# Kernel optimization log

Hardware: AMD Instinct MI355X
Metric: run time of the kernel (lower is better)

Reference implementation:

```python
import jax, jax.numpy as jnp
import numpy as np

N_NODES = 8192
SEQ = 256
H = 32  # lstm_hdim == gcn_hdim


def lstm_layer(x, Wih, Whh, bih, bhh, return_seq):
    # x: [B, S, D] -> torch nn.LSTM, gate order i,f,g,o
    B = x.shape[0]
    Hd = Whh.shape[1]
    b = bih + bhh

    def step(carry, xt):
        h, c = carry
        z = xt @ Wih.T + h @ Whh.T + b  # [B, 4H]
        i, f, g, o = jnp.split(z, 4, axis=-1)
        c = jax.nn.sigmoid(f) * c + jax.nn.sigmoid(i) * jnp.tanh(g)
        h = jax.nn.sigmoid(o) * jnp.tanh(c)
        return (h, c), (h if return_seq else None)

    init = (jnp.zeros((B, Hd), x.dtype), jnp.zeros((B, Hd), x.dtype))
    (h_n, _), ys = jax.lax.scan(step, init, jnp.transpose(x, (1, 0, 2)))
    if return_seq:
        ys = jnp.transpose(ys, (1, 0, 2))  # [B, S, H]
    return ys, h_n


def layer_norm(x, g, b, eps=1e-5):
    mu = jnp.mean(x, axis=-1, keepdims=True)
    var = jnp.mean((x - mu) ** 2, axis=-1, keepdims=True)
    return (x - mu) * jax.lax.rsqrt(var + eps) * g + b


def gcn_conv(x, edge_index, edge_weight, W, bias, n_nodes):
    # PyG GCNConv with self-loops (fill 1.0) and symmetric normalization.
    h = x @ W  # transform first (in_dim -> out_dim)
    src, dst = edge_index[0], edge_index[1]
    deg = jax.ops.segment_sum(edge_weight, dst, num_segments=n_nodes) + 1.0  # +1 self loop
    dinv = jnp.where(deg > 0, jax.lax.rsqrt(deg), 0.0)
    norm = dinv[src] * edge_weight * dinv[dst]  # [E]
    agg = jax.ops.segment_sum(norm[:, None] * h[src], dst, num_segments=n_nodes)
    agg = agg + h * (dinv * dinv)[:, None]  # self-loop message
    return agg + bias


def setup_inputs() -> dict:
    key = jax.random.key(0)
    ks = jax.random.split(key, 20)
    s = 0.1
    d = {
        "x": jax.random.normal(ks[0], (N_NODES, SEQ), jnp.float32),
        "edge_weight": jax.random.uniform(ks[1], (262144,), jnp.float32),
        "Wih1": jax.random.normal(ks[2], (4 * H, 1)) * s,
        "Whh1": jax.random.normal(ks[3], (4 * H, H)) * s,
        "bih1": jax.random.normal(ks[4], (4 * H,)) * s,
        "bhh1": jax.random.normal(ks[5], (4 * H,)) * s,
        "ln1_g": jnp.ones((H,), jnp.float32),
        "ln1_b": jnp.zeros((H,), jnp.float32),
        "Wih2": jax.random.normal(ks[6], (4 * H, H)) * s,
        "Whh2": jax.random.normal(ks[7], (4 * H, H)) * s,
        "bih2": jax.random.normal(ks[8], (4 * H,)) * s,
        "bhh2": jax.random.normal(ks[9], (4 * H,)) * s,
        "Wg1": jax.random.normal(ks[10], (H, H)) * s,
        "bg1": jax.random.normal(ks[11], (H,)) * s,
        "Wg2": jax.random.normal(ks[12], (H, H)) * s,
        "bg2": jax.random.normal(ks[13], (H,)) * s,
        "Wfc": jax.random.normal(ks[14], (2, H + 1)) * s,
        "bfc": jax.random.normal(ks[15], (2,)) * s,
        "edge_index": jax.random.randint(ks[16], (2, 262144), 0, N_NODES, jnp.int64 if jax.config.jax_enable_x64 else jnp.int32),
    }
    return d


def reference(x, edge_weight, Wih1, Whh1, bih1, bhh1, ln1_g, ln1_b,
              Wih2, Whh2, bih2, bhh2, Wg1, bg1, Wg2, bg2, Wfc, bfc, edge_index):
    n = x.shape[0]
    xs = x[:, :, None]  # [B, S, 1]
    # Temporal module (batched over all samples; dropout off in eval).
    y1, _ = lstm_layer(xs, Wih1, Whh1, bih1, bhh1, return_seq=True)
    y1 = layer_norm(y1, ln1_g, ln1_b)
    _, h2 = lstm_layer(y1, Wih2, Whh2, bih2, bhh2, return_seq=False)  # [B, H]
    gcn_in = h2  # lstm_out.view(-1, lstm_hdim)
    # Spatial module: 2 GCNConv + ELU (dropout between layers is identity in eval).
    g = jax.nn.elu(gcn_conv(gcn_in, edge_index, edge_weight, Wg1, bg1, n))
    g = jax.nn.elu(gcn_conv(g, edge_index, edge_weight, Wg2, bg2, n))
    feat = jnp.concatenate([gcn_in, jnp.mean(g, axis=1, keepdims=True)], axis=1)  # [B, H+1]
    out = feat @ Wfc.T + bfc
    return jax.nn.log_softmax(out, axis=1)
```

## Files before the change

kernel.cpp:

```cpp
#include <hip/hip_runtime.h>

typedef __attribute__((ext_vector_type(8))) short short8;
typedef __attribute__((ext_vector_type(4))) float float4v;

#define NNODES 8192
#define SEQLEN 256

static __device__ __forceinline__ float bf2f(unsigned short u) {
  union { unsigned u; float f; } v; v.u = ((unsigned)u) << 16; return v.f;
}
static __device__ __forceinline__ unsigned short f2bf(float f) {
  union { float f; unsigned u; } v; v.f = f;
  unsigned r = v.u + 0x7FFFu + ((v.u >> 16) & 1u);
  return (unsigned short)(r >> 16);
}
static __device__ __forceinline__ void splitbf8(const float* v, short8& hi) {
#pragma unroll
  for (int j = 0; j < 8; ++j) hi[j] = (short)f2bf(v[j]);
}

static __device__ __forceinline__ float lstm_cell(float zi, float zf, float zg,
                                                  float zo, float& c) {
  float ef = __builtin_amdgcn_exp2f(-zf);
  float ei = __builtin_amdgcn_exp2f(-zi);
  float eg = __builtin_amdgcn_exp2f(fminf(zg + zg, 60.f));
  float fterm = c * __builtin_amdgcn_rcpf(1.f + ef);
  float igt = (eg - 1.f) * __builtin_amdgcn_rcpf((1.f + ei) * (eg + 1.f));
  c = fterm + igt;
  float eo = __builtin_amdgcn_exp2f(-zo);
  float ec = __builtin_amdgcn_exp2f(fminf(2.88539008178f * c, 40.f));
  return (ec - 1.f) * __builtin_amdgcn_rcpf((1.f + eo) * (ec + 1.f));
}

__global__ __launch_bounds__(512, 4)
void lstm_fused(const float* __restrict__ x,
                const float* __restrict__ Wih1, const float* __restrict__ Whh1,
                const float* __restrict__ bih1, const float* __restrict__ bhh1,
                const float* __restrict__ ln_g, const float* __restrict__ ln_b,
                const float* __restrict__ Wih2, const float* __restrict__ Whh2,
                const float* __restrict__ bih2, const float* __restrict__ bhh2,
                const float* __restrict__ Wg1,
                float* __restrict__ h2out, float* __restrict__ hWa)
{
  const int tid = threadIdx.x;
  const int w = tid >> 6;
  const int lane = tid & 63;
  const int c = lane & 15;
  const int q = lane >> 4;
  const int cn = lane >> 2;
  const int ch = lane & 3;
  const int hid = w * 4 + ch;
  const int nodeBase = blockIdx.x * 16;
  const float L = 1.44269504089f;

  __shared__ __align__(16) float xlds[16 * 260];
  __shared__ __align__(16) float zbuf1[16 * 132];
  __shared__ __align__(16) float zbuf2[16 * 132];
  __shared__ __align__(16) unsigned short h1p[2][16 * 40];
  __shared__ __align__(16) unsigned short h2p[2][16 * 40];
  __shared__ __align__(16) float mu2[32];
  __shared__ __align__(16) float wgbuf[32 * 33];
  __shared__ __align__(16) float h2f[16 * 33];

  for (int i = tid; i < 16 * 256; i += 512) {
    int nn = i >> 8, tt = i & 255;
    xlds[nn * 260 + tt] = x[(size_t)(nodeBase + nn) * SEQLEN + tt];
  }
  if (tid < 64) xlds[(tid >> 2) * 260 + 256 + (tid & 3)] = 0.f;
  for (int i = tid; i < 1024; i += 512) wgbuf[(i >> 5) * 33 + (i & 31)] = Wg1[i];

  const int brow = (c & 3) * 32 + w * 4 + (c >> 2);
  short8 Bh1, Bi2, Bh2;
  float Gpre, b1pre, b2pre;
  {
    float v[8];
#pragma unroll
    for (int j = 0; j < 8; ++j) v[j] = L * Whh1[brow * 32 + q * 8 + j];
    splitbf8(v, Bh1);
#pragma unroll
    for (int j = 0; j < 8; ++j) v[j] = L * Wih2[brow * 32 + q * 8 + j] * ln_g[q * 8 + j];
    splitbf8(v, Bi2);
#pragma unroll
    for (int j = 0; j < 8; ++j) v[j] = L * Whh2[brow * 32 + q * 8 + j];
    splitbf8(v, Bh2);
    float sG = 0.f, sB = 0.f;
    for (int k = 0; k < 32; ++k) {
      sG += Wih2[brow * 32 + k] * ln_g[k];
      sB += Wih2[brow * 32 + k] * ln_b[k];
    }
    Gpre = L * sG;
    b1pre = L * (bih1[brow] + bhh1[brow]);
    b2pre = L * (sB + bih2[brow] + bhh2[brow]);
  }
  const float4v C1 = {b1pre, b1pre, b1pre, b1pre};
  const float4v C2 = {b2pre, b2pre, b2pre, b2pre};
  const float4v z4 = {0.f, 0.f, 0.f, 0.f};
  float w1v[4];
#pragma unroll
  for (int g = 0; g < 4; ++g) w1v[g] = L * Wih1[g * 32 + hid];

  int zW[4];
#pragma unroll
  for (int r = 0; r < 4; ++r) zW[r] = (q * 4 + r) * 132 + w * 16 + c;
  const int zR = cn * 132 + hid * 4;
  const int hWr = cn * 40 + hid;
  const int hRd = c * 40 + q * 8;

  short8 h1A = {0,0,0,0,0,0,0,0};
  short8 h2A = {0,0,0,0,0,0,0,0};
  float c1 = 0.f, c2 = 0.f, hv2 = 0.f;
  __syncthreads();

  {
    float4v za = __builtin_amdgcn_mfma_f32_16x16x32_bf16(h1A, Bh1, C1, 0, 0, 0);
#pragma unroll
    for (int r = 0; r < 4; ++r) zbuf1[zW[r]] = za[r];
    float4v zv = *(const float4v*)&zbuf1[zR];
    float xv = xlds[cn * 260 + 0];
    float hv = lstm_cell(fmaf(xv, w1v[0], zv[0]), fmaf(xv, w1v[1], zv[1]),
                         fmaf(xv, w1v[2], zv[2]), fmaf(xv, w1v[3], zv[3]), c1);
    h1p[1][hWr] = f2bf(hv);
  }
  __syncthreads();
  h1A = *(const short8*)&h1p[1][hRd];

  for (int t = 0; t < SEQLEN; ++t) {
    const int pl = t & 1;
    float4v za = __builtin_amdgcn_mfma_f32_16x16x32_bf16(h1A, Bh1, C1, 0, 0, 0);
    float4v db = __builtin_amdgcn_mfma_f32_16x16x32_bf16(h2A, Bh2, C2, 0, 0, 0);

    float s = 0.f, s2 = 0.f;
#pragma unroll
    for (int j = 0; j < 8; ++j) {
      float hf = bf2f((unsigned short)h1A[j]);
      s += hf; s2 = fmaf(hf, hf, s2);
    }
    s  += __shfl_xor(s, 16, 64);  s  += __shfl_xor(s, 32, 64);
    s2 += __shfl_xor(s2, 16, 64); s2 += __shfl_xor(s2, 32, 64);
    float mu = s * (1.f / 32.f);
    float var = s2 * (1.f / 32.f) - mu * mu;
    float rstd = rsqrtf(var + 1e-5f);
    if (q < 2) mu2[c * 2 + q] = (q == 0) ? rstd : rstd * mu;

    float4v da = __builtin_amdgcn_mfma_f32_16x16x32_bf16(h1A, Bi2, z4, 0, 0, 0);
#pragma unroll
    for (int r = 0; r < 4; ++r) {
      float2 ab = *(const float2*)&mu2[(q * 4 + r) * 2];
      zbuf2[zW[r]] = fmaf(ab.x, da[r], fmaf(-ab.y, Gpre, db[r]));
      zbuf1[zW[r]] = za[r];
    }
    {
      float4v zv = *(const float4v*)&zbuf2[zR];
      hv2 = lstm_cell(zv[0], zv[1], zv[2], zv[3], c2);
      h2p[pl][hWr] = f2bf(hv2);
    }
    {
      float4v zv = *(const float4v*)&zbuf1[zR];
      float xv = xlds[cn * 260 + t + 1];
      float hv = lstm_cell(fmaf(xv, w1v[0], zv[0]), fmaf(xv, w1v[1], zv[1]),
                           fmaf(xv, w1v[2], zv[2]), fmaf(xv, w1v[3], zv[3]), c1);
      h1p[pl][hWr] = f2bf(hv);
    }
    __syncthreads();
    h1A = *(const short8*)&h1p[pl][hRd];
    h2A = *(const short8*)&h2p[pl][hRd];
  }

  h2out[(size_t)(nodeBase + cn) * 32 + hid] = hv2;

  __syncthreads();
  h2f[cn * 33 + hid] = hv2;
  __syncthreads();
  {
    int nl = tid >> 5, j = tid & 31;
    float acc = 0.f;
#pragma unroll
    for (int k = 0; k < 32; ++k) acc = fmaf(h2f[nl * 33 + k], wgbuf[k * 33 + j], acc);
    hWa[(size_t)(nodeBase + nl) * 32 + j] = acc;
  }
}

__global__ void count_k(const int* __restrict__ ei, const float* __restrict__ ew,
                        unsigned long long* __restrict__ pk, int E) {
  int e = blockIdx.x * 256 + threadIdx.x;
  if (e >= E) return;
  int d = ei[E + e];
  unsigned long long pay = (1ull << 40) |
      (unsigned long long)(unsigned)(ew[e] * 16777216.f + 0.5f);
  atomicAdd(&pk[d], pay);
}

__global__ __launch_bounds__(1024, 1)
void scan_k(const unsigned long long* __restrict__ pk, int* __restrict__ off,
            int* __restrict__ pos, float* __restrict__ dinv) {
  __shared__ int wtot[16];
  __shared__ int wexcl[16];
  int tid = threadIdx.x;
  int wv = tid >> 6, lane = tid & 63;
  int base = tid * 8;
  int v[8]; int sum = 0;
#pragma unroll
  for (int i = 0; i < 8; ++i) {
    unsigned long long u = pk[base + i];
    v[i] = (int)(u >> 40);
    float degv = (float)(u & 0xFFFFFFFFFFull) * (1.f / 16777216.f);
    dinv[base + i] = rsqrtf(degv + 1.0f);
    sum += v[i];
  }
  int incl = sum;
#pragma unroll
  for (int d = 1; d < 64; d <<= 1) {
    int t = __shfl_up(incl, d, 64);
    if (lane >= d) incl += t;
  }
  if (lane == 63) wtot[wv] = incl;
  __syncthreads();
  if (wv == 0 && lane < 16) {
    int wval = wtot[lane];
    int wincl = wval;
#pragma unroll
    for (int d = 1; d < 16; d <<= 1) {
      int t = __shfl_up(wincl, d, 64);
      if (lane >= d) wincl += t;
    }
    wexcl[lane] = wincl - wval;
  }
  __syncthreads();
  int run = wexcl[wv] + (incl - sum);
#pragma unroll
  for (int i = 0; i < 8; ++i) {
    off[base + i] = run; pos[base + i] = run; run += v[i];
  }
  if (tid == 1023) off[8192] = run;
}

__global__ void scatter_k(const int* __restrict__ ei, const float* __restrict__ ew,
                          const float* __restrict__ dinv, int* __restrict__ pos,
                          int2* __restrict__ ed, int E) {
  int e = blockIdx.x * 256 + threadIdx.x;
  if (e >= E) return;
  int sidx = ei[e], d = ei[E + e];
  int p = atomicAdd(&pos[d], 1);
  int2 pay;
  pay.x = sidx;
  pay.y = __float_as_int(dinv[sidx] * ew[e] * dinv[d]);
  ed[p] = pay;
}

__global__ __launch_bounds__(512, 4)
void gather_mid_k(const int* __restrict__ off, const int2* __restrict__ ed,
                  const float* __restrict__ dinv, const float* __restrict__ hWa,
                  const float* __restrict__ bg1, const float* __restrict__ Wg2,
                  float* __restrict__ aggB) {
  __shared__ float wg[32 * 33];
  __shared__ float g1buf[16][33];
  int tid = threadIdx.x;
  for (int i = tid; i < 1024; i += 512) wg[(i >> 5) * 33 + (i & 31)] = Wg2[i];
  int nl = tid >> 5, j = tid & 31;
  int node = blockIdx.x * 16 + nl;
  float dv = dinv[node];
  float a0 = dv * dv * hWa[(size_t)node * 32 + j];
  float a1 = 0.f, a2 = 0.f, a3 = 0.f;
  int p0 = off[node], p1 = off[node + 1];
  int p = p0;
  for (; p + 3 < p1; p += 4) {
    int2 e0 = ed[p], e1 = ed[p + 1], e2 = ed[p + 2], e3 = ed[p + 3];
    a0 = fmaf(__int_as_float(e0.y), hWa[(size_t)e0.x * 32 + j], a0);
    a1 = fmaf(__int_as_float(e1.y), hWa[(size_t)e1.x * 32 + j], a1);
    a2 = fmaf(__int_as_float(e2.y), hWa[(size_t)e2.x * 32 + j], a2);
    a3 = fmaf(__int_as_float(e3.y), hWa[(size_t)e3.x * 32 + j], a3);
  }
  for (; p < p1; ++p) {
    int2 e0 = ed[p];
    a0 = fmaf(__int_as_float(e0.y), hWa[(size_t)e0.x * 32 + j], a0);
  }
  float v = (a0 + a1) + (a2 + a3) + bg1[j];
  g1buf[nl][j] = (v > 0.f) ? v : expm1f(v);
  __syncthreads();
  float acc = 0.f;
#pragma unroll
  for (int k = 0; k < 32; ++k) acc = fmaf(g1buf[nl][k], wg[k * 33 + j], acc);
  aggB[(size_t)node * 32 + j] = acc;
}

__global__ __launch_bounds__(512, 4)
void gather_final_k(const int* __restrict__ off, const int2* __restrict__ ed,
                    const float* __restrict__ dinv, const float* __restrict__ aggB,
                    const float* __restrict__ bg2, const float* __restrict__ h2o,
                    const float* __restrict__ Wfc, const float* __restrict__ bfc,
                    float* __restrict__ out) {
  int tid = threadIdx.x;
  int nl = tid >> 5, j = tid & 31;
  int node = blockIdx.x * 16 + nl;
  float dv = dinv[node];
  float a0 = dv * dv * aggB[(size_t)node * 32 + j];
  float a1 = 0.f, a2 = 0.f, a3 = 0.f;
  int p0 = off[node], p1 = off[node + 1];
  int p = p0;
  for (; p + 3 < p1; p += 4) {
    int2 e0 = ed[p], e1 = ed[p + 1], e2 = ed[p + 2], e3 = ed[p + 3];
    a0 = fmaf(__int_as_float(e0.y), aggB[(size_t)e0.x * 32 + j], a0);
    a1 = fmaf(__int_as_float(e1.y), aggB[(size_t)e1.x * 32 + j], a1);
    a2 = fmaf(__int_as_float(e2.y), aggB[(size_t)e2.x * 32 + j], a2);
    a3 = fmaf(__int_as_float(e3.y), aggB[(size_t)e3.x * 32 + j], a3);
  }
  for (; p < p1; ++p) {
    int2 e0 = ed[p];
    a0 = fmaf(__int_as_float(e0.y), aggB[(size_t)e0.x * 32 + j], a0);
  }
  float v = (a0 + a1) + (a2 + a3) + bg2[j];
  float e = (v > 0.f) ? v : expm1f(v);
  float h2v = h2o[(size_t)node * 32 + j];
  float p0s = h2v * Wfc[j];
  float p1s = h2v * Wfc[33 + j];
#pragma unroll
  for (int m = 1; m < 32; m <<= 1) {
    e   += __shfl_xor(e, m, 32);
    p0s += __shfl_xor(p0s, m, 32);
    p1s += __shfl_xor(p1s, m, 32);
  }
  if (j == 0) {
    float mean = e * (1.f / 32.f);
    float o0 = p0s + mean * Wfc[32] + bfc[0];
    float o1 = p1s + mean * Wfc[65] + bfc[1];
    float mx = fmaxf(o0, o1);
    float l = mx + logf(expf(o0 - mx) + expf(o1 - mx));
    out[node * 2 + 0] = o0 - l;
    out[node * 2 + 1] = o1 - l;
  }
}

extern "C" void kernel_launch(void* const* d_in, const int* in_sizes, int n_in,
                              void* d_out, int out_size, void* d_ws, size_t ws_size,
                              hipStream_t stream) {
  const float* x    = (const float*)d_in[0];
  const float* ew   = (const float*)d_in[1];
  const float* Wih1 = (const float*)d_in[2];
  const float* Whh1 = (const float*)d_in[3];
  const float* bih1 = (const float*)d_in[4];
  const float* bhh1 = (const float*)d_in[5];
  const float* ln_g = (const float*)d_in[6];
  const float* ln_b = (const float*)d_in[7];
  const float* Wih2 = (const float*)d_in[8];
  const float* Whh2 = (const float*)d_in[9];
  const float* bih2 = (const float*)d_in[10];
  const float* bhh2 = (const float*)d_in[11];
  const float* Wg1  = (const float*)d_in[12];
  const float* bg1  = (const float*)d_in[13];
  const float* Wg2  = (const float*)d_in[14];
  const float* bg2  = (const float*)d_in[15];
  const float* Wfc  = (const float*)d_in[16];
  const float* bfc  = (const float*)d_in[17];
  const int* ei     = (const int*)d_in[18];
  float* out = (float*)d_out;
  const int E = in_sizes[1];

  float* ws   = (float*)d_ws;
  float* h2o  = ws;
  float* hWa  = ws + 262144;
  float* aggB = ws + 524288;
  unsigned long long* pk = (unsigned long long*)(ws + 786432);
  float* dinv = ws + 802816;
  int*   off  = (int*)(ws + 811008);
  int*   pos  = (int*)(ws + 819208);
  int2*  ed   = (int2*)(ws + 827400);

  hipMemsetAsync((void*)pk, 0, 8192 * sizeof(unsigned long long), stream);
  hipLaunchKernelGGL(count_k, dim3((E + 255) / 256), dim3(256), 0, stream, ei, ew, pk, E);
  hipLaunchKernelGGL(lstm_fused, dim3(NNODES / 16), dim3(512), 0, stream,
                     x, Wih1, Whh1, bih1, bhh1, ln_g, ln_b,
                     Wih2, Whh2, bih2, bhh2, Wg1, h2o, hWa);
  hipLaunchKernelGGL(scan_k, dim3(1), dim3(1024), 0, stream, pk, off, pos, dinv);
  hipLaunchKernelGGL(scatter_k, dim3((E + 255) / 256), dim3(256), 0, stream, ei, ew, dinv, pos, ed, E);
  hipLaunchKernelGGL(gather_mid_k, dim3(NNODES / 16), dim3(512), 0, stream,
                     off, ed, dinv, hWa, bg1, Wg2, aggB);
  hipLaunchKernelGGL(gather_final_k, dim3(NNODES / 16), dim3(512), 0, stream,
                     off, ed, dinv, aggB, bg2, h2o, Wfc, bfc, out);
}
```

Before: 435.0 us.

## Fuse LSTM and GCN pipeline into one cooperative kernel with grid syncs

Replaces the six separate kernel launches (edge count, LSTM, scan, scatter, two gathers) with a single cooperative mega-kernel that separates phases with grid-wide synchronization. This removes inter-kernel launch gaps and tail effects. In exchange, the serial scan phase runs on one block while all others wait at a grid barrier, and edge counting no longer overlaps the LSTM. It falls back to the old multi-kernel path if the cooperative launch fails.

```diff
diff --git a/kernel.cpp b/kernel.cpp
--- a/kernel.cpp
+++ b/kernel.cpp
@@ -1,4 +1,7 @@
 #include <hip/hip_runtime.h>
+#include <hip/hip_cooperative_groups.h>
+
+namespace cg = cooperative_groups;
 
 typedef __attribute__((ext_vector_type(8))) short short8;
 typedef __attribute__((ext_vector_type(4))) float float4v;
@@ -18,7 +21,6 @@
 #pragma unroll
   for (int j = 0; j < 8; ++j) hi[j] = (short)f2bf(v[j]);
 }
-
 static __device__ __forceinline__ float lstm_cell(float zi, float zf, float zg,
                                                   float zo, float& c) {
   float ef = __builtin_amdgcn_exp2f(-zf);
@@ -30,6 +32,292 @@
   float eo = __builtin_amdgcn_exp2f(-zo);
   float ec = __builtin_amdgcn_exp2f(fminf(2.88539008178f * c, 40.f));
   return (ec - 1.f) * __builtin_amdgcn_rcpf((1.f + eo) * (ec + 1.f));
+}
+
+struct MArgs {
+  const float *x, *Wih1, *Whh1, *bih1, *bhh1, *ln_g, *ln_b, *Wih2, *Whh2, *bih2, *bhh2;
+  const float *Wg1, *bg1, *Wg2, *bg2, *Wfc, *bfc, *ew;
+  const int* ei;
+  unsigned long long* pk;
+  float *dinv, *h2o, *hWa, *aggB, *out;
+  int *off, *pos;
+  int2* ed;
+  int E;
+};
+
+__global__ __launch_bounds__(512, 4) void mega_k(MArgs a) {
+  cg::grid_group grid = cg::this_grid();
+  const int tid = threadIdx.x;
+  const int w = tid >> 6;
+  const int lane = tid & 63;
+  const int c = lane & 15;
+  const int q = lane >> 4;
+  const int cn = lane >> 2;
+  const int ch = lane & 3;
+  const int hid = w * 4 + ch;
+  const int nodeBase = blockIdx.x * 16;
+  const float L = 1.44269504089f;
+
+  __shared__ __align__(16) float xlds[16 * 260];
+  __shared__ __align__(16) float zbuf1[16 * 132];
+  __shared__ __align__(16) float zbuf2[16 * 132];
+  __shared__ __align__(16) unsigned short h1p[2][16 * 40];
+  __shared__ __align__(16) unsigned short h2p[2][16 * 40];
+  __shared__ __align__(16) float mu2[32];
+  __shared__ __align__(16) float wgbuf[32 * 33];
+  __shared__ __align__(16) float h2f[16 * 33];
+  __shared__ int wtot[8], wexcl[8];
+
+  for (int i = tid; i < 16 * 256; i += 512) {
+    int nn = i >> 8, tt = i & 255;
+    xlds[nn * 260 + tt] = a.x[(size_t)(nodeBase + nn) * SEQLEN + tt];
+  }
+  if (tid < 64) xlds[(tid >> 2) * 260 + 256 + (tid & 3)] = 0.f;
+  for (int i = tid; i < 1024; i += 512) wgbuf[(i >> 5) * 33 + (i & 31)] = a.Wg1[i];
+
+  const int brow = (c & 3) * 32 + w * 4 + (c >> 2);
+  short8 Bh1, Bi2, Bh2;
+  float Gpre, b1pre, b2pre;
+  {
+    float v[8];
+#pragma unroll
+    for (int j = 0; j < 8; ++j) v[j] = L * a.Whh1[brow * 32 + q * 8 + j];
+    splitbf8(v, Bh1);
+#pragma unroll
+    for (int j = 0; j < 8; ++j) v[j] = L * a.Wih2[brow * 32 + q * 8 + j] * a.ln_g[q * 8 + j];
+    splitbf8(v, Bi2);
+#pragma unroll
+    for (int j = 0; j < 8; ++j) v[j] = L * a.Whh2[brow * 32 + q * 8 + j];
+    splitbf8(v, Bh2);
+    float sG = 0.f, sB = 0.f;
+    for (int k = 0; k < 32; ++k) {
+      sG += a.Wih2[brow * 32 + k] * a.ln_g[k];
+      sB += a.Wih2[brow * 32 + k] * a.ln_b[k];
+    }
+    Gpre = L * sG;
+    b1pre = L * (a.bih1[brow] + a.bhh1[brow]);
+    b2pre = L * (sB + a.bih2[brow] + a.bhh2[brow]);
+  }
+  const float4v C1 = {b1pre, b1pre, b1pre, b1pre};
+  const float4v C2 = {b2pre, b2pre, b2pre, b2pre};
+  const float4v z4 = {0.f, 0.f, 0.f, 0.f};
+  float w1v[4];
+#pragma unroll
+  for (int g = 0; g < 4; ++g) w1v[g] = L * a.Wih1[g * 32 + hid];
+
+  int zW[4];
+#pragma unroll
+  for (int r = 0; r < 4; ++r) zW[r] = (q * 4 + r) * 132 + w * 16 + c;
+  const int zR = cn * 132 + hid * 4;
+  const int hWr = cn * 40 + hid;
+  const int hRd = c * 40 + q * 8;
+
+  short8 h1A = {0,0,0,0,0,0,0,0};
+  short8 h2A = {0,0,0,0,0,0,0,0};
+  float c1 = 0.f, c2 = 0.f, hv2 = 0.f;
+  __syncthreads();
+
+  {
+    float4v za = __builtin_amdgcn_mfma_f32_16x16x32_bf16(h1A, Bh1, C1, 0, 0, 0);
+#pragma unroll
+    for (int r = 0; r < 4; ++r) zbuf1[zW[r]] = za[r];
+    float4v zv = *(const float4v*)&zbuf1[zR];
+    float xv = xlds[cn * 260 + 0];
+    float hv = lstm_cell(fmaf(xv, w1v[0], zv[0]), fmaf(xv, w1v[1], zv[1]),
+                         fmaf(xv, w1v[2], zv[2]), fmaf(xv, w1v[3], zv[3]), c1);
+    h1p[1][hWr] = f2bf(hv);
+  }
+  __syncthreads();
+  h1A = *(const short8*)&h1p[1][hRd];
+
+  for (int t = 0; t < SEQLEN; ++t) {
+    const int pl = t & 1;
+    float4v za = __builtin_amdgcn_mfma_f32_16x16x32_bf16(h1A, Bh1, C1, 0, 0, 0);
+    float4v db = __builtin_amdgcn_mfma_f32_16x16x32_bf16(h2A, Bh2, C2, 0, 0, 0);
+
+    float s = 0.f, s2 = 0.f;
+#pragma unroll
+    for (int j = 0; j < 8; ++j) {
+      float hf = bf2f((unsigned short)h1A[j]);
+      s += hf; s2 = fmaf(hf, hf, s2);
+    }
+    s  += __shfl_xor(s, 16, 64);  s  += __shfl_xor(s, 32, 64);
+    s2 += __shfl_xor(s2, 16, 64); s2 += __shfl_xor(s2, 32, 64);
+    float mu = s * (1.f / 32.f);
+    float var = s2 * (1.f / 32.f) - mu * mu;
+    float rstd = rsqrtf(var + 1e-5f);
+    if (q < 2) mu2[c * 2 + q] = (q == 0) ? rstd : rstd * mu;
+
+    float4v da = __builtin_amdgcn_mfma_f32_16x16x32_bf16(h1A, Bi2, z4, 0, 0, 0);
+#pragma unroll
+    for (int r = 0; r < 4; ++r) {
+      float2 ab = *(const float2*)&mu2[(q * 4 + r) * 2];
+      zbuf2[zW[r]] = fmaf(ab.x, da[r], fmaf(-ab.y, Gpre, db[r]));
+      zbuf1[zW[r]] = za[r];
+    }
+    {
+      float4v zv = *(const float4v*)&zbuf2[zR];
+      hv2 = lstm_cell(zv[0], zv[1], zv[2], zv[3], c2);
+      h2p[pl][hWr] = f2bf(hv2);
+    }
+    {
+      float4v zv = *(const float4v*)&zbuf1[zR];
+      float xv = xlds[cn * 260 + t + 1];
+      float hv = lstm_cell(fmaf(xv, w1v[0], zv[0]), fmaf(xv, w1v[1], zv[1]),
+                           fmaf(xv, w1v[2], zv[2]), fmaf(xv, w1v[3], zv[3]), c1);
+      h1p[pl][hWr] = f2bf(hv);
+    }
+    __syncthreads();
+    h1A = *(const short8*)&h1p[pl][hRd];
+    h2A = *(const short8*)&h2p[pl][hRd];
+  }
+
+  a.h2o[(size_t)(nodeBase + cn) * 32 + hid] = hv2;
+
+  __syncthreads();
+  h2f[cn * 33 + hid] = hv2;
+  __syncthreads();
+  {
+    int nl = tid >> 5, j = tid & 31;
+    float acc = 0.f;
+#pragma unroll
+    for (int k = 0; k < 32; ++k) acc = fmaf(h2f[nl * 33 + k], wgbuf[k * 33 + j], acc);
+    a.hWa[(size_t)(nodeBase + nl) * 32 + j] = acc;
+  }
+
+  {
+    int e = blockIdx.x * 512 + tid;
+    if (e < a.E) {
+      int d = a.ei[a.E + e];
+      unsigned long long pay = (1ull << 40) |
+          (unsigned long long)(unsigned)(a.ew[e] * 16777216.f + 0.5f);
+      atomicAdd(&a.pk[d], pay);
+    }
+  }
+  grid.sync();
+
+  if (blockIdx.x == 0) {
+    int base = tid * 16;
+    int v[16]; int sum = 0;
+#pragma unroll
+    for (int i = 0; i < 16; ++i) {
+      unsigned long long u = a.pk[base + i];
+      v[i] = (int)(u >> 40);
+      float degv = (float)(u & 0xFFFFFFFFFFull) * (1.f / 16777216.f);
+      a.dinv[base + i] = rsqrtf(degv + 1.0f);
+      sum += v[i];
+    }
+    int incl = sum;
+#pragma unroll
+    for (int d = 1; d < 64; d <<= 1) {
+      int t = __shfl_up(incl, d, 64);
+      if (lane >= d) incl += t;
+    }
+    if (lane == 63) wtot[w] = incl;
+    __syncthreads();
+    if (w == 0 && lane < 8) {
+      int wval = wtot[lane];
+      int wincl = wval;
+#pragma unroll
+      for (int d = 1; d < 8; d <<= 1) {
+        int t = __shfl_up(wincl, d, 64);
+        if (lane >= d) wincl += t;
+      }
+      wexcl[lane] = wincl - wval;
+    }
+    __syncthreads();
+    int run = wexcl[w] + (incl - sum);
+#pragma unroll
+    for (int i = 0; i < 16; ++i) {
+      a.off[base + i] = run; a.pos[base + i] = run; run += v[i];
+    }
+    if (tid == 511) a.off[8192] = run;
+  }
+  grid.sync();
+
+  {
+    int e = blockIdx.x * 512 + tid;
+    if (e < a.E) {
+      int sidx = a.ei[e], d = a.ei[a.E + e];
+      int p = atomicAdd(&a.pos[d], 1);
+      int2 pay;
+      pay.x = sidx;
+      pay.y = __float_as_int(a.dinv[sidx] * a.ew[e] * a.dinv[d]);
+      a.ed[p] = pay;
+    }
+  }
+  grid.sync();
+
+  {
+    for (int i = tid; i < 1024; i += 512) wgbuf[(i >> 5) * 33 + (i & 31)] = a.Wg2[i];
+    int nl = tid >> 5, j = tid & 31;
+    int node = blockIdx.x * 16 + nl;
+    float dv = a.dinv[node];
+    float a0 = dv * dv * a.hWa[(size_t)node * 32 + j];
+    float a1 = 0.f, a2 = 0.f, a3 = 0.f;
+    int p0 = a.off[node], p1 = a.off[node + 1];
+    int p = p0;
+    for (; p + 3 < p1; p += 4) {
+      int2 e0 = a.ed[p], e1 = a.ed[p + 1], e2 = a.ed[p + 2], e3 = a.ed[p + 3];
+      a0 = fmaf(__int_as_float(e0.y), a.hWa[(size_t)e0.x * 32 + j], a0);
+      a1 = fmaf(__int_as_float(e1.y), a.hWa[(size_t)e1.x * 32 + j], a1);
+      a2 = fmaf(__int_as_float(e2.y), a.hWa[(size_t)e2.x * 32 + j], a2);
+      a3 = fmaf(__int_as_float(e3.y), a.hWa[(size_t)e3.x * 32 + j], a3);
+    }
+    for (; p < p1; ++p) {
+      int2 e0 = a.ed[p];
+      a0 = fmaf(__int_as_float(e0.y), a.hWa[(size_t)e0.x * 32 + j], a0);
+    }
+    float v = (a0 + a1) + (a2 + a3) + a.bg1[j];
+    h2f[nl * 33 + j] = (v > 0.f) ? v : expm1f(v);
+    __syncthreads();
+    float acc = 0.f;
+#pragma unroll
+    for (int k = 0; k < 32; ++k) acc = fmaf(h2f[nl * 33 + k], wgbuf[k * 33 + j], acc);
+    a.aggB[(size_t)node * 32 + j] = acc;
+  }
+  grid.sync();
+
+  {
+    int nl = tid >> 5, j = tid & 31;
+    int node = blockIdx.x * 16 + nl;
+    float dv = a.dinv[node];
+    float a0 = dv * dv * a.aggB[(size_t)node * 32 + j];
+    float a1 = 0.f, a2 = 0.f, a3 = 0.f;
+    int p0 = a.off[node], p1 = a.off[node + 1];
+    int p = p0;
+    for (; p + 3 < p1; p += 4) {
+      int2 e0 = a.ed[p], e1 = a.ed[p + 1], e2 = a.ed[p + 2], e3 = a.ed[p + 3];
+      a0 = fmaf(__int_as_float(e0.y), a.aggB[(size_t)e0.x * 32 + j], a0);
+      a1 = fmaf(__int_as_float(e1.y), a.aggB[(size_t)e1.x * 32 + j], a1);
+      a2 = fmaf(__int_as_float(e2.y), a.aggB[(size_t)e2.x * 32 + j], a2);
+      a3 = fmaf(__int_as_float(e3.y), a.aggB[(size_t)e3.x * 32 + j], a3);
+    }
+    for (; p < p1; ++p) {
+      int2 e0 = a.ed[p];
+      a0 = fmaf(__int_as_float(e0.y), a.aggB[(size_t)e0.x * 32 + j], a0);
+    }
+    float v = (a0 + a1) + (a2 + a3) + a.bg2[j];
+    float e = (v > 0.f) ? v : expm1f(v);
+    float h2v = a.h2o[(size_t)node * 32 + j];
+    float p0s = h2v * a.Wfc[j];
+    float p1s = h2v * a.Wfc[33 + j];
+#pragma unroll
+    for (int m = 1; m < 32; m <<= 1) {
+      e   += __shfl_xor(e, m, 32);
+      p0s += __shfl_xor(p0s, m, 32);
+      p1s += __shfl_xor(p1s, m, 32);
+    }
+    if (j == 0) {
+      float mean = e * (1.f / 32.f);
+      float o0 = p0s + mean * a.Wfc[32] + a.bfc[0];
+      float o1 = p1s + mean * a.Wfc[65] + a.bfc[1];
+      float mx = fmaxf(o0, o1);
+      float l = mx + logf(expf(o0 - mx) + expf(o1 - mx));
+      a.out[node * 2 + 0] = o0 - l;
+      a.out[node * 2 + 1] = o1 - l;
+    }
+  }
 }
 
 __global__ __launch_bounds__(512, 4)
@@ -366,14 +654,29 @@
   int2*  ed   = (int2*)(ws + 827400);
 
   hipMemsetAsync((void*)pk, 0, 8192 * sizeof(unsigned long long), stream);
-  hipLaunchKernelGGL(count_k, dim3((E + 255) / 256), dim3(256), 0, stream, ei, ew, pk, E);
-  hipLaunchKernelGGL(lstm_fused, dim3(NNODES / 16), dim3(512), 0, stream,
-                     x, Wih1, Whh1, bih1, bhh1, ln_g, ln_b,
-                     Wih2, Whh2, bih2, bhh2, Wg1, h2o, hWa);
-  hipLaunchKernelGGL(scan_k, dim3(1), dim3(1024), 0, stream, pk, off, pos, dinv);
-  hipLaunchKernelGGL(scatter_k, dim3((E + 255) / 256), dim3(256), 0, stream, ei, ew, dinv, pos, ed, E);
-  hipLaunchKernelGGL(gather_mid_k, dim3(NNODES / 16), dim3(512), 0, stream,
-                     off, ed, dinv, hWa, bg1, Wg2, aggB);
-  hipLaunchKernelGGL(gather_final_k, dim3(NNODES / 16), dim3(512), 0, stream,
-                     off, ed, dinv, aggB, bg2, h2o, Wfc, bfc, out);
-}
+
+  MArgs m;
+  m.x = x; m.Wih1 = Wih1; m.Whh1 = Whh1; m.bih1 = bih1; m.bhh1 = bhh1;
+  m.ln_g = ln_g; m.ln_b = ln_b; m.Wih2 = Wih2; m.Whh2 = Whh2;
+  m.bih2 = bih2; m.bhh2 = bhh2; m.Wg1 = Wg1; m.bg1 = bg1; m.Wg2 = Wg2;
+  m.bg2 = bg2; m.Wfc = Wfc; m.bfc = bfc; m.ew = ew; m.ei = ei;
+  m.pk = pk; m.dinv = dinv; m.h2o = h2o; m.hWa = hWa; m.aggB = aggB;
+  m.out = out; m.off = off; m.pos = pos; m.ed = ed; m.E = E;
+
+  void* kargs[] = { (void*)&m };
+  hipError_t err = hipLaunchCooperativeKernel((const void*)mega_k, dim3(NNODES / 16),
+                                              dim3(512), kargs, 0, stream);
+  if (err != hipSuccess) {
+    (void)hipGetLastError();
+    hipLaunchKernelGGL(count_k, dim3((E + 255) / 256), dim3(256), 0, stream, ei, ew, pk, E);
+    hipLaunchKernelGGL(lstm_fused, dim3(NNODES / 16), dim3(512), 0, stream,
+                       x, Wih1, Whh1, bih1, bhh1, ln_g, ln_b,
+                       Wih2, Whh2, bih2, bhh2, Wg1, h2o, hWa);
+    hipLaunchKernelGGL(scan_k, dim3(1), dim3(1024), 0, stream, pk, off, pos, dinv);
+    hipLaunchKernelGGL(scatter_k, dim3((E + 255) / 256), dim3(256), 0, stream, ei, ew, dinv, pos, ed, E);
+    hipLaunchKernelGGL(gather_mid_k, dim3(NNODES / 16), dim3(512), 0, stream,
+                       off, ed, dinv, hWa, bg1, Wg2, aggB);
+    hipLaunchKernelGGL(gather_final_k, dim3(NNODES / 16), dim3(512), 0, stream,
+                       off, ed, dinv, aggB, bg2, h2o, Wfc, bfc, out);
+  }
+}
```

Result: slower. 674.3 us (+55.0%).
